# Optimization experiments

Measured on AMD Instinct MI355X. Metric: run time of the kernel, lower is better.

## Reference

```python
import jax, jax.numpy as jnp
import numpy as np

B_, L, DM = 2, 2048, 1024
DI, N, K, R = 2048, 16, 4, 64  # d_inner, d_state, d_conv, dt_rank


def setup_inputs() -> dict:
    key = jax.random.key(0)
    ks = jax.random.split(key, 8)
    return {
        "x": jax.random.normal(ks[0], (B_, L, DM), jnp.float32),
        "W_in": jax.random.normal(ks[1], (DM, 2 * DI), jnp.float32) * 0.02,
        "w_conv": jax.random.normal(ks[2], (DI, K), jnp.float32) * 0.1,
        "b_conv": jnp.zeros((DI,), jnp.float32),
        "W_x": jax.random.normal(ks[3], (DI, R + 2 * N), jnp.float32) * 0.02,
        "W_dt": jax.random.normal(ks[4], (R, DI), jnp.float32) * 0.02,
        "b_dt": jnp.full((DI,), -4.6, jnp.float32),  # softplus(b_dt) ~ 0.01 dt init
        "A_log": jnp.log(jnp.broadcast_to(jnp.arange(1, N + 1, dtype=jnp.float32), (DI, N))),
        "D": jnp.ones((DI,), jnp.float32),
        "W_out": jax.random.normal(ks[5], (DI, DM), jnp.float32) * 0.02,
        "gamma": jnp.ones((DM,), jnp.float32),
        "beta": jnp.zeros((DM,), jnp.float32),
    }


def reference(x, W_in, w_conv, b_conv, W_x, W_dt, b_dt, A_log, D, W_out, gamma, beta):
    Bb, Ll, Dm = x.shape
    Di, Kk = w_conv.shape
    Nn = A_log.shape[1]
    Rr = W_dt.shape[0]
    # in_proj -> (u, z)
    xz = x @ W_in  # [B,L,2*Di]
    u, z = jnp.split(xz, 2, axis=-1)
    # depthwise causal conv1d (kernel K, left pad K-1) + SiLU
    up = jnp.pad(u, ((0, 0), (Kk - 1, 0), (0, 0)))
    conv = b_conv + sum(up[:, k:k + Ll, :] * w_conv[:, k] for k in range(Kk))
    u = jax.nn.silu(conv)  # [B,L,Di]
    # x_proj -> dt, B, C
    dbc = u @ W_x
    dt, Bm, Cm = dbc[..., :Rr], dbc[..., Rr:Rr + Nn], dbc[..., Rr + Nn:]
    delta = jax.nn.softplus(dt @ W_dt + b_dt)  # [B,L,Di]
    A = -jnp.exp(A_log)  # [Di,N]

    def step(h, inputs):
        d_t, B_t, C_t, u_t = inputs  # [B,Di],[B,N],[B,N],[B,Di]
        dA = jnp.exp(d_t[..., None] * A)            # [B,Di,N]
        h = h * dA + (d_t * u_t)[..., None] * B_t[:, None, :]
        y = jnp.einsum('bdn,bn->bd', h, C_t)
        return h, y

    h0 = jnp.zeros((Bb, Di, Nn), x.dtype)
    _, ys = jax.lax.scan(step, h0, (delta.transpose(1, 0, 2), Bm.transpose(1, 0, 2),
                                    Cm.transpose(1, 0, 2), u.transpose(1, 0, 2)))
    y = ys.transpose(1, 0, 2)        # [B,L,Di]
    y = y + u * D                    # skip term
    y = y * jax.nn.silu(z)           # gate
    out = y @ W_out                  # [B,L,Dm]
    # LayerNorm
    mu = out.mean(-1, keepdims=True)
    var = ((out - mu) ** 2).mean(-1, keepdims=True)
    out = (out - mu) * jax.lax.rsqrt(var + 1e-5) * gamma + beta
    # dropout p=0 -> identity; residual
    return out + x
```

## Files before the change

kernel.cpp:

```cpp
#include <hip/hip_runtime.h>
#include <math.h>

#define L_SEQ 2048
#define DMOD  1024
#define DIN   2048
#define NBATCH 2
#define NTOK  (NBATCH * L_SEQ)
#define NST   16
#define RRANK 64
#define LOG2E 1.44269504088896f

#define GCHUNK 64
#define CLEN   (L_SEQ / GCHUNK)
#define SCHUNK 8
#define NSTAGE (CLEN / SCHUNK)

#define G4_KS   4
#define G4_KC   (2048 / G4_KS)
#define G2_KS   16
#define G2_KC   (2048 / G2_KS)

typedef __attribute__((ext_vector_type(8))) short  short8;
typedef __attribute__((ext_vector_type(4))) float  f32x4;

__device__ __forceinline__ ushort f2bf(float f) {
    unsigned u = __float_as_uint(f);
    u += 0x7fffu + ((u >> 16) & 1u);
    return (ushort)(u >> 16);
}
__device__ __forceinline__ float bf2f(ushort u) {
    return __uint_as_float(((unsigned)u) << 16);
}
__device__ __forceinline__ float fexp2(float x) {
    return __builtin_amdgcn_exp2f(x);
}

__device__ __forceinline__ void gload16(const ushort* g, ushort* l) {
    __builtin_amdgcn_global_load_lds(
        (const __attribute__((address_space(1))) unsigned int*)g,
        (__attribute__((address_space(3))) unsigned int*)l,
        16, 0, 0);
}

__device__ __forceinline__ void cast_body(
    const float* __restrict__ src, ushort* __restrict__ dst, int bid, int tid)
{
    int i = (bid * 256 + tid) * 8;
    float4 a = *(const float4*)(src + i);
    float4 b = *(const float4*)(src + i + 4);
    ushort4 o0 = make_ushort4(f2bf(a.x), f2bf(a.y), f2bf(a.z), f2bf(a.w));
    ushort4 o1 = make_ushort4(f2bf(b.x), f2bf(b.y), f2bf(b.z), f2bf(b.w));
    *(ushort4*)(dst + i)     = o0;
    *(ushort4*)(dst + i + 4) = o1;
}

__device__ __forceinline__ void tcast_body(
    const float* __restrict__ src, ushort* __restrict__ dst,
    int R, int C, int bx, int by, int tid)
{
    __shared__ float t[32][33];
    int tx = tid & 31;
    int ty = tid >> 5;
    int c0 = bx * 32;
    int r0 = by * 32;
    #pragma unroll
    for (int i = 0; i < 4; ++i)
        t[ty + i * 8][tx] = src[(size_t)(r0 + ty + i * 8) * C + c0 + tx];
    __syncthreads();
    #pragma unroll
    for (int i = 0; i < 4; ++i)
        dst[(size_t)(c0 + ty + i * 8) * R + r0 + tx] = f2bf(t[tx][ty + i * 8]);
}

__global__ __launch_bounds__(256) void prep_k(
    const float* __restrict__ x, const float* __restrict__ W_in,
    const float* __restrict__ W_dt, const float* __restrict__ W_x,
    const float* __restrict__ W_out,
    ushort* __restrict__ xb, ushort* __restrict__ Wib,
    ushort* __restrict__ Wdtb, ushort* __restrict__ Wxb,
    ushort* __restrict__ Wob)
{
    int bid = blockIdx.x, tid = threadIdx.x;
    if (bid < 2048) {
        cast_body(x, xb, bid, tid);
    } else if (bid < 6144) {
        int t = bid - 2048;
        tcast_body(W_in, Wib, 1024, 4096, t & 127, t >> 7, tid);
    } else if (bid < 6272) {
        int t = bid - 6144;
        tcast_body(W_dt, Wdtb, 64, 2048, t & 63, t >> 6, tid);
    } else if (bid < 6464) {
        int t = bid - 6272;
        tcast_body(W_x, Wxb, 2048, 96, t % 3, t / 3, tid);
    } else {
        int t = bid - 6464;
        tcast_body(W_out, Wob, 2048, 1024, t & 31, t >> 5, tid);
    }
}

__global__ __launch_bounds__(512, 2) void gemm8p(
    const ushort* __restrict__ A,
    const ushort* __restrict__ Bt,
    ushort* __restrict__ C,
    int K, int kslice, int ldc, size_t zstride)
{
    __shared__ ushort As[4][8192];
    __shared__ ushort Bs[4][8192];

    const int tid  = threadIdx.x;
    const int wave = tid >> 6;
    const int lane = tid & 63;
    const int wr   = wave >> 2;
    const int wc   = wave & 3;

    const int gx = gridDim.x;
    int flat = blockIdx.y * gx + blockIdx.x;
    const int cpx = (gx * gridDim.y) >> 3;
    flat = (flat & 7) * cpx + (flat >> 3);
    const int bx = flat % gx;
    const int by = flat / gx;
    const int m0 = by * 256;
    const int n0 = bx * 256;
    const int kbeg = blockIdx.z * kslice;
    const int NS   = kslice >> 5;

    const int rr  = tid >> 2;
    const int gsw = ((tid & 3) ^ ((rr >> 1) & 3)) * 8;
    const ushort* a0 = A  + (size_t)(m0 + rr)        * K + kbeg + gsw;
    const ushort* a1 = A  + (size_t)(m0 + 128 + rr)  * K + kbeg + gsw;
    const ushort* b0 = Bt + (size_t)(n0 + rr)        * K + kbeg + gsw;
    const ushort* b1 = Bt + (size_t)(n0 + 128 + rr)  * K + kbeg + gsw;
    ushort* asw = &As[0][0] + wave * 512;
    ushort* bsw = &Bs[0][0] + wave * 512;

    #define STAGE(s_) do { const int sl_ = (s_) & 3; const int ko_ = (s_) * 32; \
        gload16(a0 + ko_, asw + sl_ * 8192);                                     \
        gload16(a1 + ko_, asw + sl_ * 8192 + 4096);                              \
        gload16(b0 + ko_, bsw + sl_ * 8192);                                     \
        gload16(b1 + ko_, bsw + sl_ * 8192 + 4096); } while (0)

    const int lr  = lane & 15;
    const int swr = ((lane >> 4) ^ ((lr >> 1) & 3)) * 8;

    f32x4 acc[8][4];
    #pragma unroll
    for (int i = 0; i < 8; ++i)
        #pragma unroll
        for (int j = 0; j < 4; ++j)
            acc[i][j] = (f32x4){0.f, 0.f, 0.f, 0.f};

    STAGE(0); STAGE(1); STAGE(2);

    for (int s = 0; s < NS; ++s) {
        if (s + 2 < NS)
            asm volatile("s_waitcnt vmcnt(8) lgkmcnt(0)" ::: "memory");
        else if (s + 1 < NS)
            asm volatile("s_waitcnt vmcnt(4) lgkmcnt(0)" ::: "memory");
        else
            asm volatile("s_waitcnt vmcnt(0) lgkmcnt(0)" ::: "memory");
        asm volatile("s_barrier" ::: "memory");
        if (s + 3 < NS) STAGE(s + 3);

        const ushort* Ab = &As[s & 3][0];
        const ushort* Bb = &Bs[s & 3][0];
        short8 af[8], bfr[4];
        #pragma unroll
        for (int j = 0; j < 4; ++j)
            bfr[j] = *(const short8*)&Bb[(wc * 64 + j * 16 + lr) * 32 + swr];
        #pragma unroll
        for (int i = 0; i < 8; ++i)
            af[i] = *(const short8*)&Ab[(wr * 128 + i * 16 + lr) * 32 + swr];

        __builtin_amdgcn_s_setprio(1);
        #pragma unroll
        for (int i = 0; i < 8; ++i)
            #pragma unroll
            for (int j = 0; j < 4; ++j)
                acc[i][j] = __builtin_amdgcn_mfma_f32_16x16x32_bf16(
                    af[i], bfr[j], acc[i][j], 0, 0, 0);
        __builtin_amdgcn_s_setprio(0);
    }
    #undef STAGE

    ushort* Cp = C + (size_t)blockIdx.z * zstride;
    const int rb = m0 + wr * 128 + ((lane >> 4) << 2);
    const int cb = n0 + wc * 64 + lr;
    #pragma unroll
    for (int i = 0; i < 8; ++i)
        #pragma unroll
        for (int j = 0; j < 4; ++j)
            #pragma unroll
            for (int r = 0; r < 4; ++r)
                Cp[(size_t)(rb + i * 16 + r) * ldc + cb + j * 16] =
                    f2bf(acc[i][j][r]);
}

template<int EPI, int OBF>
__global__ __launch_bounds__(256) void gemm_mfma(
    const ushort* __restrict__ A,
    const ushort* __restrict__ Bt,
    void* __restrict__ Cv,
    int M, int N, int K, int ldc, const float* __restrict__ bias)
{
    __shared__ ushort As[128 * 32];
    __shared__ ushort Bs[128 * 32];

    const int tid  = threadIdx.x;
    const int wave = tid >> 6;
    const int lane = tid & 63;
    const int wm   = (wave & 1) * 64;
    const int wn   = (wave >> 1) * 64;
    const int m0   = blockIdx.y * 128;
    const int n0   = blockIdx.x * 128;

    const int srow = lane >> 2;
    const int sg   = (lane & 3) ^ ((srow >> 1) & 3);
    const ushort* gA0 = A  + (size_t)(m0 + wave * 32 + srow)      * K + sg * 8;
    const ushort* gA1 = A  + (size_t)(m0 + wave * 32 + 16 + srow) * K + sg * 8;
    const ushort* gB0 = Bt + (size_t)(n0 + wave * 32 + srow)      * K + sg * 8;
    const ushort* gB1 = Bt + (size_t)(n0 + wave * 32 + 16 + srow) * K + sg * 8;
    ushort* lA0 = As + (wave * 32)      * 32;
    ushort* lA1 = As + (wave * 32 + 16) * 32;
    ushort* lB0 = Bs + (wave * 32)      * 32;
    ushort* lB1 = Bs + (wave * 32 + 16) * 32;

    const int lrow = lane & 15;
    const int swr  = ((lane >> 4) ^ ((lrow >> 1) & 3)) * 8;

    f32x4 acc[4][4];
    #pragma unroll
    for (int i = 0; i < 4; ++i)
        #pragma unroll
        for (int j = 0; j < 4; ++j)
            acc[i][j] = (f32x4){0.f, 0.f, 0.f, 0.f};

    for (int k0 = 0; k0 < K; k0 += 32) {
        __syncthreads();
        gload16(gA0 + k0, lA0);
        gload16(gA1 + k0, lA1);
        gload16(gB0 + k0, lB0);
        gload16(gB1 + k0, lB1);
        __syncthreads();

        short8 af[4], bfr[4];
        #pragma unroll
        for (int i = 0; i < 4; ++i) {
            af[i]  = *(const short8*)&As[(wm + i * 16 + lrow) * 32 + swr];
            bfr[i] = *(const short8*)&Bs[(wn + i * 16 + lrow) * 32 + swr];
        }
        #pragma unroll
        for (int i = 0; i < 4; ++i)
            #pragma unroll
            for (int j = 0; j < 4; ++j)
                acc[i][j] = __builtin_amdgcn_mfma_f32_16x16x32_bf16(
                    af[i], bfr[j], acc[i][j], 0, 0, 0);
    }

    const int rb = m0 + wm + ((lane >> 4) << 2);
    const int cb = n0 + wn + lrow;
    #pragma unroll
    for (int i = 0; i < 4; ++i)
        #pragma unroll
        for (int j = 0; j < 4; ++j)
            #pragma unroll
            for (int r = 0; r < 4; ++r) {
                float v = acc[i][j][r];
                int col = cb + j * 16;
                if (EPI == 1) {
                    v += bias[col];
                    v = (v > 20.f) ? v : log1pf(__expf(v));
                }
                size_t off = (size_t)(rb + i * 16 + r) * ldc + col;
                if (OBF) ((ushort*)Cv)[off] = f2bf(v);
                else     ((float*)Cv)[off]  = v;
            }
}

__global__ __launch_bounds__(256) void gemm2_mfma(
    const ushort* __restrict__ A,
    const ushort* __restrict__ Bt,
    float* __restrict__ part)
{
    __shared__ ushort As[128 * 32];
    __shared__ ushort Bs[128 * 32];

    const int K = 2048;
    const int tid  = threadIdx.x;
    const int wave = tid >> 6;
    const int lane = tid & 63;
    const int wm   = (wave & 1) * 64;
    const int wn   = (wave >> 1) * 64;
    const int m0   = blockIdx.x * 128;
    const int ks   = blockIdx.z;

    const int srow = lane >> 2;
    const int sg   = (lane & 3) ^ ((srow >> 1) & 3);
    int rB0 = wave * 32 + srow;      if (rB0 > 95) rB0 = 95;
    int rB1 = wave * 32 + 16 + srow; if (rB1 > 95) rB1 = 95;
    const ushort* gA0 = A  + (size_t)(m0 + wave * 32 + srow)      * K + sg * 8;
    const ushort* gA1 = A  + (size_t)(m0 + wave * 32 + 16 + srow) * K + sg * 8;
    const ushort* gB0 = Bt + (size_t)rB0 * K + sg * 8;
    const ushort* gB1 = Bt + (size_t)rB1 * K + sg * 8;
    ushort* lA0 = As + (wave * 32)      * 32;
    ushort* lA1 = As + (wave * 32 + 16) * 32;
    ushort* lB0 = Bs + (wave * 32)      * 32;
    ushort* lB1 = Bs + (wave * 32 + 16) * 32;

    const int lrow = lane & 15;
    const int swr  = ((lane >> 4) ^ ((lrow >> 1) & 3)) * 8;

    f32x4 acc[4][4];
    #pragma unroll
    for (int i = 0; i < 4; ++i)
        #pragma unroll
        for (int j = 0; j < 4; ++j)
            acc[i][j] = (f32x4){0.f, 0.f, 0.f, 0.f};

    const int kbeg = ks * G2_KC, kend = kbeg + G2_KC;
    for (int k0 = kbeg; k0 < kend; k0 += 32) {
        __syncthreads();
        gload16(gA0 + k0, lA0);
        gload16(gA1 + k0, lA1);
        gload16(gB0 + k0, lB0);
        gload16(gB1 + k0, lB1);
        __syncthreads();

        short8 af[4], bfr[4];
        #pragma unroll
        for (int i = 0; i < 4; ++i) {
            af[i]  = *(const short8*)&As[(wm + i * 16 + lrow) * 32 + swr];
            bfr[i] = *(const short8*)&Bs[(wn + i * 16 + lrow) * 32 + swr];
        }
        #pragma unroll
        for (int i = 0; i < 4; ++i)
            #pragma unroll
            for (int j = 0; j < 4; ++j)
                acc[i][j] = __builtin_amdgcn_mfma_f32_16x16x32_bf16(
                    af[i], bfr[j], acc[i][j], 0, 0, 0);
    }

    float* po = part + (size_t)ks * NTOK * 96;
    const int rb = m0 + wm + ((lane >> 4) << 2);
    const int cb = wn + lrow;
    #pragma unroll
    for (int i = 0; i < 4; ++i)
        #pragma unroll
        for (int j = 0; j < 4; ++j) {
            int col = cb + j * 16;
            if (col < 96) {
                #pragma unroll
                for (int r = 0; r < 4; ++r)
                    po[(size_t)(rb + i * 16 + r) * 96 + col] = acc[i][j][r];
            }
        }
}

__global__ __launch_bounds__(256) void gemm2_reduce_dt(
    const float* __restrict__ part, float* __restrict__ dbc,
    ushort* __restrict__ dtb)
{
    int i = (blockIdx.x * 256 + threadIdx.x) * 4;
    float4 s = *(const float4*)(part + i);
    #pragma unroll
    for (int ks = 1; ks < G2_KS; ++ks) {
        float4 v = *(const float4*)(part + (size_t)ks * NTOK * 96 + i);
        s.x += v.x; s.y += v.y; s.z += v.z; s.w += v.w;
    }
    *(float4*)(dbc + i) = s;
    int col = i % 96;
    if (col < RRANK) {
        int row = i / 96;
        ushort* q = dtb + (size_t)row * RRANK + col;
        q[0] = f2bf(s.x); q[1] = f2bf(s.y); q[2] = f2bf(s.z); q[3] = f2bf(s.w);
    }
}

__global__ __launch_bounds__(256) void conv_silu_k(
    const ushort* __restrict__ xzb, const float* __restrict__ w_conv,
    const float* __restrict__ b_conv, ushort* __restrict__ ub)
{
    int idx   = blockIdx.x * 256 + threadIdx.x;
    int d     = idx & (DIN - 1);
    int token = idx >> 11;
    int t     = token & (L_SEQ - 1);

    float acc = b_conv[d];
    #pragma unroll
    for (int k = 0; k < 4; ++k) {
        int tt = t - 3 + k;
        if (tt >= 0)
            acc += bf2f(xzb[(size_t)(token - 3 + k) * 4096 + d]) * w_conv[d * 4 + k];
    }
    float s = acc / (1.f + expf(-acc));
    ub[(size_t)token * DIN + d] = f2bf(s);
}

__global__ __launch_bounds__(64) void scan_part1(
    const float* __restrict__ dlt,
    const ushort* __restrict__ ub,
    const float* __restrict__ dbc,
    const float* __restrict__ A_log,
    float* __restrict__ c_out,
    float* __restrict__ dsum_out)
{
    int chunk = blockIdx.x & 63;
    int dg    = (blockIdx.x >> 6) & 31;
    int b     = blockIdx.x >> 11;
    int tid   = threadIdx.x;
    int d     = dg * 64 + tid;

    __shared__ float sB[SCHUNK][16];

    float Al[NST];
    const float4* pA = (const float4*)(A_log + (size_t)d * NST);
    #pragma unroll
    for (int q = 0; q < 4; ++q) {
        float4 a = pA[q];
        Al[q*4+0] = -__expf(a.x) * LOG2E;
        Al[q*4+1] = -__expf(a.y) * LOG2E;
        Al[q*4+2] = -__expf(a.z) * LOG2E;
        Al[q*4+3] = -__expf(a.w) * LOG2E;
    }

    float h[NST];
    #pragma unroll
    for (int n = 0; n < NST; ++n) h[n] = 0.f;
    float dsum = 0.f;

    const size_t tokbase = (size_t)b * L_SEQ + (size_t)chunk * CLEN;
    const float*  pD = dlt + tokbase * 2048 + d;
    const ushort* pU = ub  + tokbase * 2048 + d;
    const float*  pB = dbc + tokbase * 96 + RRANK;

    float rd[2][SCHUNK], ru[2][SCHUNK], rb[2][2];

    #pragma unroll
    for (int i = 0; i < SCHUNK; ++i) {
        rd[0][i] = pD[(size_t)i * 2048];
        ru[0][i] = bf2f(pU[(size_t)i * 2048]);
    }
    #pragma unroll
    for (int i = 0; i < 2; ++i) {
        int e = i * 64 + tid;
        rb[0][i] = pB[(size_t)(e >> 4) * 96 + (e & 15)];
    }

    #pragma unroll
    for (int st = 0; st < NSTAGE; ++st) {
        const int cur = st & 1, nxt = cur ^ 1;
        #pragma unroll
        for (int i = 0; i < 2; ++i) {
            int e = i * 64 + tid;
            sB[e >> 4][e & 15] = rb[cur][i];
        }
        if (st + 1 < NSTAGE) {
            const size_t to = (size_t)(st + 1) * SCHUNK;
            #pragma unroll
            for (int i = 0; i < SCHUNK; ++i) {
                rd[nxt][i] = pD[(to + i) * 2048];
                ru[nxt][i] = bf2f(pU[(to + i) * 2048]);
            }
            #pragma unroll
            for (int i = 0; i < 2; ++i) {
                int e = i * 64 + tid;
                rb[nxt][i] = pB[(to + (e >> 4)) * 96 + (e & 15)];
            }
        }
        #pragma unroll
        for (int s = 0; s < SCHUNK; ++s) {
            float delta = rd[cur][s];
            float du    = delta * ru[cur][s];
            dsum += delta;
            #pragma unroll
            for (int q = 0; q < 4; ++q) {
                float4 bq = *(const float4*)&sB[s][q * 4];
                h[q*4+0] = h[q*4+0] * fexp2(delta * Al[q*4+0]) + du * bq.x;
                h[q*4+1] = h[q*4+1] * fexp2(delta * Al[q*4+1]) + du * bq.y;
                h[q*4+2] = h[q*4+2] * fexp2(delta * Al[q*4+2]) + du * bq.z;
                h[q*4+3] = h[q*4+3] * fexp2(delta * Al[q*4+3]) + du * bq.w;
            }
        }
    }

    size_t base = (((size_t)b * DIN + d) * GCHUNK + chunk) * NST;
    #pragma unroll
    for (int q = 0; q < 4; ++q)
        *(float4*)&c_out[base + q * 4] = make_float4(h[q*4], h[q*4+1], h[q*4+2], h[q*4+3]);
    dsum_out[((size_t)b * DIN + d) * GCHUNK + chunk] = dsum;
}

__global__ __launch_bounds__(256) void scan_part2(
    float* __restrict__ cbuf,
    const float* __restrict__ dsum_in,
    const float* __restrict__ A_log)
{
    int idx = blockIdx.x * 256 + threadIdx.x;
    int n   = idx & 15;
    int d   = (idx >> 4) & (DIN - 1);
    int b   = idx >> 15;

    float Al = -__expf(A_log[(size_t)d * NST + n]) * LOG2E;
    size_t cb = ((size_t)b * DIN + d) * GCHUNK;

    float h = 0.f;
    for (int ch = 0; ch < GCHUNK; ++ch) {
        size_t o = (cb + ch) * NST + n;
        float c  = cbuf[o];
        float dA = fexp2(Al * dsum_in[cb + ch]);
        cbuf[o]  = h;
        h = h * dA + c;
    }
}

__global__ __launch_bounds__(64) void scan_part3(
    const float* __restrict__ dlt,
    const ushort* __restrict__ xzb,
    ushort* __restrict__ ub,
    const float* __restrict__ dbc,
    const float* __restrict__ A_log,
    const float* __restrict__ Dp,
    const float* __restrict__ h_start)
{
    int chunk = blockIdx.x & 63;
    int dg    = (blockIdx.x >> 6) & 31;
    int b     = blockIdx.x >> 11;
    int tid   = threadIdx.x;
    int d     = dg * 64 + tid;

    __shared__ float sBC[SCHUNK][32];

    float Al[NST];
    const float4* pA = (const float4*)(A_log + (size_t)d * NST);
    #pragma unroll
    for (int q = 0; q < 4; ++q) {
        float4 a = pA[q];
        Al[q*4+0] = -__expf(a.x) * LOG2E;
        Al[q*4+1] = -__expf(a.y) * LOG2E;
        Al[q*4+2] = -__expf(a.z) * LOG2E;
        Al[q*4+3] = -__expf(a.w) * LOG2E;
    }
    float Dd = Dp[d];

    float h[NST];
    size_t hb = (((size_t)b * DIN + d) * GCHUNK + chunk) * NST;
    #pragma unroll
    for (int q = 0; q < 4; ++q) {
        float4 v = *(const float4*)&h_start[hb + q * 4];
        h[q*4] = v.x; h[q*4+1] = v.y; h[q*4+2] = v.z; h[q*4+3] = v.w;
    }

    const size_t tokbase = (size_t)b * L_SEQ + (size_t)chunk * CLEN;
    const float*  pD = dlt + tokbase * 2048 + d;
    const ushort* pZ = xzb + tokbase * 4096 + 2048 + d;
    ushort*       pU = ub  + tokbase * 2048 + d;
    const float*  pB = dbc + tokbase * 96 + RRANK;

    float rd[2][SCHUNK], ru[2][SCHUNK], rz[2][SCHUNK], rb[2][4];

    #pragma unroll
    for (int i = 0; i < SCHUNK; ++i) {
        rd[0][i] = pD[(size_t)i * 2048];
        ru[0][i] = bf2f(pU[(size_t)i * 2048]);
        rz[0][i] = bf2f(pZ[(size_t)i * 4096]);
    }
    #pragma unroll
    for (int i = 0; i < 4; ++i) {
        int e = i * 64 + tid;
        rb[0][i] = pB[(size_t)(e >> 5) * 96 + (e & 31)];
    }

    #pragma unroll
    for (int st = 0; st < NSTAGE; ++st) {
        const int cur = st & 1, nxt = cur ^ 1;
        #pragma unroll
        for (int i = 0; i < 4; ++i) {
            int e = i * 64 + tid;
            sBC[e >> 5][e & 31] = rb[cur][i];
        }
        if (st + 1 < NSTAGE) {
            const size_t to = (size_t)(st + 1) * SCHUNK;
            #pragma unroll
            for (int i = 0; i < SCHUNK; ++i) {
                rd[nxt][i] = pD[(to + i) * 2048];
                ru[nxt][i] = bf2f(pU[(to + i) * 2048]);
                rz[nxt][i] = bf2f(pZ[(to + i) * 4096]);
            }
            #pragma unroll
            for (int i = 0; i < 4; ++i) {
                int e = i * 64 + tid;
                rb[nxt][i] = pB[(to + (e >> 5)) * 96 + (e & 31)];
            }
        }
        #pragma unroll
        for (int s = 0; s < SCHUNK; ++s) {
            float delta = rd[cur][s];
            float u     = ru[cur][s];
            float du    = delta * u;
            float y = 0.f;
            #pragma unroll
            for (int q = 0; q < 4; ++q) {
                float4 bq = *(const float4*)&sBC[s][q * 4];
                float4 cq = *(const float4*)&sBC[s][16 + q * 4];
                h[q*4+0] = h[q*4+0] * fexp2(delta * Al[q*4+0]) + du * bq.x; y += h[q*4+0] * cq.x;
                h[q*4+1] = h[q*4+1] * fexp2(delta * Al[q*4+1]) + du * bq.y; y += h[q*4+1] * cq.y;
                h[q*4+2] = h[q*4+2] * fexp2(delta * Al[q*4+2]) + du * bq.z; y += h[q*4+2] * cq.z;
                h[q*4+3] = h[q*4+3] * fexp2(delta * Al[q*4+3]) + du * bq.w; y += h[q*4+3] * cq.w;
            }
            float z  = rz[cur][s];
            float sz = z / (1.f + __expf(-z));
            pU[((size_t)st * SCHUNK + s) * 2048] = f2bf((y + u * Dd) * sz);
        }
    }
}

__global__ __launch_bounds__(256) void ln4_k(
    const ushort* __restrict__ part,
    const float* __restrict__ x,
    const float* __restrict__ gamma, const float* __restrict__ beta,
    float* __restrict__ out)
{
    int row = blockIdx.x;
    int tid = threadIdx.x;
    const size_t off = (size_t)row * DMOD + tid * 4;

    float4 v = {0.f, 0.f, 0.f, 0.f};
    #pragma unroll
    for (int ks = 0; ks < G4_KS; ++ks) {
        ushort4 p = *(const ushort4*)(part + (size_t)ks * NTOK * DMOD + off);
        v.x += bf2f(p.x); v.y += bf2f(p.y); v.z += bf2f(p.z); v.w += bf2f(p.w);
    }

    float s  = v.x + v.y + v.z + v.w;
    float s2 = v.x * v.x + v.y * v.y + v.z * v.z + v.w * v.w;
    #pragma unroll
    for (int off2 = 32; off2 > 0; off2 >>= 1) {
        s  += __shfl_down(s, off2);
        s2 += __shfl_down(s2, off2);
    }
    __shared__ float ws[4], ws2[4];
    int wave = tid >> 6, lane = tid & 63;
    if (lane == 0) { ws[wave] = s; ws2[wave] = s2; }
    __syncthreads();
    if (tid == 0) {
        float ts = 0.f, ts2 = 0.f;
        #pragma unroll
        for (int w = 0; w < 4; ++w) { ts += ws[w]; ts2 += ws2[w]; }
        ws[0] = ts; ws2[0] = ts2;
    }
    __syncthreads();
    float mu  = ws[0] * (1.f / DMOD);
    float var = ws2[0] * (1.f / DMOD) - mu * mu;
    float rs  = rsqrtf(var + 1e-5f);

    float4 g  = ((const float4*)gamma)[tid];
    float4 be = ((const float4*)beta)[tid];
    float4 xr = *(const float4*)(x + off);
    float4 o;
    o.x = (v.x - mu) * rs * g.x + be.x + xr.x;
    o.y = (v.y - mu) * rs * g.y + be.y + xr.y;
    o.z = (v.z - mu) * rs * g.z + be.z + xr.z;
    o.w = (v.w - mu) * rs * g.w + be.w + xr.w;
    *(float4*)(out + off) = o;
}

extern "C" void kernel_launch(void* const* d_in, const int* in_sizes, int n_in,
                              void* d_out, int out_size, void* d_ws, size_t ws_size,
                              hipStream_t stream)
{
    const float* x      = (const float*)d_in[0];
    const float* W_in   = (const float*)d_in[1];
    const float* w_conv = (const float*)d_in[2];
    const float* b_conv = (const float*)d_in[3];
    const float* W_x    = (const float*)d_in[4];
    const float* W_dt   = (const float*)d_in[5];
    const float* b_dt   = (const float*)d_in[6];
    const float* A_log  = (const float*)d_in[7];
    const float* Dp     = (const float*)d_in[8];
    const float* W_out  = (const float*)d_in[9];
    const float* gamma  = (const float*)d_in[10];
    const float* beta   = (const float*)d_in[11];
    float* out = (float*)d_out;

    char* ws = (char*)d_ws;
    const size_t MB = 1024 * 1024;
    ushort* xzb   = (ushort*)(ws);
    ushort* ub    = (ushort*)(ws + 32 * MB);
    float*  dlt   = (float*)(ws + 48 * MB);
    float*  dbc   = (float*)(ws + 80 * MB);
    ushort* Wdtb  = (ushort*)(ws + 81 * MB + 512 * 1024);
    ushort* Wxb   = (ushort*)(ws + 81 * MB + 768 * 1024);
    float*  dsum  = (float*)(ws + 82 * MB + 256 * 1024);
    float*  c_buf = (float*)(ws + 84 * MB);
    ushort* xb    = (ushort*)(ws + 84 * MB);
    ushort* Wib   = (ushort*)(ws + 92 * MB);
    float*  g2part = (float*)(ws + 84 * MB);
    ushort* dtb   = (ushort*)(ws + 108 * MB);
    ushort* Wob   = (ushort*)(ws + 109 * MB);
    ushort* g4part = (ushort*)(ws + 48 * MB);

    dim3 blk(256);

    prep_k<<<dim3(8512), blk, 0, stream>>>(x, W_in, W_dt, W_x, W_out,
                                           xb, Wib, Wdtb, Wxb, Wob);
    gemm8p<<<dim3(16, 16, 1), dim3(512), 0, stream>>>(
        xb, Wib, xzb, 1024, 1024, 4096, 0);
    conv_silu_k<<<dim3(NTOK * DIN / 256), blk, 0, stream>>>(xzb, w_conv, b_conv, ub);
    gemm2_mfma<<<dim3(32, 1, G2_KS), blk, 0, stream>>>(ub, Wxb, g2part);
    gemm2_reduce_dt<<<dim3(NTOK * 96 / 4 / 256), blk, 0, stream>>>(g2part, dbc, dtb);
    gemm_mfma<1, 0><<<dim3(16, 32), blk, 0, stream>>>(
        dtb, Wdtb, dlt, 4096, 2048, 64, 2048, b_dt);
    scan_part1<<<dim3(NBATCH * 32 * GCHUNK), dim3(64), 0, stream>>>(
        dlt, ub, dbc, A_log, c_buf, dsum);
    scan_part2<<<dim3(NBATCH * DIN * NST / 256), blk, 0, stream>>>(
        c_buf, dsum, A_log);
    scan_part3<<<dim3(NBATCH * 32 * GCHUNK), dim3(64), 0, stream>>>(
        dlt, xzb, ub, dbc, A_log, Dp, c_buf);
    gemm8p<<<dim3(4, 16, G4_KS), dim3(512), 0, stream>>>(
        ub, Wob, g4part, 2048, G4_KC, DMOD, (size_t)NTOK * DMOD);
    ln4_k<<<dim3(NTOK), blk, 0, stream>>>(g4part, x, gamma, beta, out);
}
```

Before: 352.4 us.

## Restructure 256x256 bf16 GEMM mainloop into double-buffered 64-K tiles with interleaved loads

Replaces the 4-slot, 32-wide K pipeline in gemm8p with a two-buffer scheme over 64-wide K tiles. Each tile is split into four phases that interleave LDS fragment reads, global-to-LDS staging of the next tile, and half-tile MFMA blocks, separated by explicit barriers and sched_barriers. Holding only half the A fragments at a time lowers register pressure. The aim is to overlap memory traffic with MFMA issue in a ping-pong style, at the cost of many more barriers per tile. The global load swizzle also changes, and it must still match the LDS read swizzle.

```diff
diff --git a/kernel.cpp b/kernel.cpp
--- a/kernel.cpp
+++ b/kernel.cpp
@@ -104,8 +104,7 @@
     ushort* __restrict__ C,
     int K, int kslice, int ldc, size_t zstride)
 {
-    __shared__ ushort As[4][8192];
-    __shared__ ushort Bs[4][8192];
+    __shared__ ushort lds[65536];
 
     const int tid  = threadIdx.x;
     const int wave = tid >> 6;
@@ -122,26 +121,31 @@
     const int m0 = by * 256;
     const int n0 = bx * 256;
     const int kbeg = blockIdx.z * kslice;
-    const int NS   = kslice >> 5;
+    const int NT   = kslice >> 6;
 
     const int rr  = tid >> 2;
-    const int gsw = ((tid & 3) ^ ((rr >> 1) & 3)) * 8;
+    const int gsw = ((tid & 3) ^ ((tid >> 3) & 3)) * 8;
     const ushort* a0 = A  + (size_t)(m0 + rr)        * K + kbeg + gsw;
     const ushort* a1 = A  + (size_t)(m0 + 128 + rr)  * K + kbeg + gsw;
     const ushort* b0 = Bt + (size_t)(n0 + rr)        * K + kbeg + gsw;
     const ushort* b1 = Bt + (size_t)(n0 + 128 + rr)  * K + kbeg + gsw;
-    ushort* asw = &As[0][0] + wave * 512;
-    ushort* bsw = &Bs[0][0] + wave * 512;
-
-    #define STAGE(s_) do { const int sl_ = (s_) & 3; const int ko_ = (s_) * 32; \
-        gload16(a0 + ko_, asw + sl_ * 8192);                                     \
-        gload16(a1 + ko_, asw + sl_ * 8192 + 4096);                              \
-        gload16(b0 + ko_, bsw + sl_ * 8192);                                     \
-        gload16(b1 + ko_, bsw + sl_ * 8192 + 4096); } while (0)
+
+    #define STAGE_U(op_, ks_, kt_, bf_) do {                                   \
+        const int ko_ = (kt_) * 64 + (ks_) * 32;                               \
+        ushort* l_ = lds + (bf_) * 32768 + (op_) * 16384 + (ks_) * 8192        \
+                         + wave * 512;                                         \
+        if ((op_) == 0) { gload16(a0 + ko_, l_); gload16(a1 + ko_, l_ + 4096); }\
+        else            { gload16(b0 + ko_, l_); gload16(b1 + ko_, l_ + 4096); }\
+    } while (0)
 
     const int lr  = lane & 15;
     const int swr = ((lane >> 4) ^ ((lr >> 1) & 3)) * 8;
 
+    #define LDA(i_, ks_) (*(const short8*)&lds[buf * 32768 + (ks_) * 8192      \
+        + (wr * 128 + (i_) * 16 + lr) * 32 + swr])
+    #define LDB(j_, ks_) (*(const short8*)&lds[buf * 32768 + 16384             \
+        + (ks_) * 8192 + (wc * 64 + (j_) * 16 + lr) * 32 + swr])
+
     f32x4 acc[8][4];
     #pragma unroll
     for (int i = 0; i < 8; ++i)
@@ -149,38 +153,96 @@
         for (int j = 0; j < 4; ++j)
             acc[i][j] = (f32x4){0.f, 0.f, 0.f, 0.f};
 
-    STAGE(0); STAGE(1); STAGE(2);
-
-    for (int s = 0; s < NS; ++s) {
-        if (s + 2 < NS)
-            asm volatile("s_waitcnt vmcnt(8) lgkmcnt(0)" ::: "memory");
-        else if (s + 1 < NS)
-            asm volatile("s_waitcnt vmcnt(4) lgkmcnt(0)" ::: "memory");
-        else
-            asm volatile("s_waitcnt vmcnt(0) lgkmcnt(0)" ::: "memory");
-        asm volatile("s_barrier" ::: "memory");
-        if (s + 3 < NS) STAGE(s + 3);
-
-        const ushort* Ab = &As[s & 3][0];
-        const ushort* Bb = &Bs[s & 3][0];
-        short8 af[8], bfr[4];
-        #pragma unroll
-        for (int j = 0; j < 4; ++j)
-            bfr[j] = *(const short8*)&Bb[(wc * 64 + j * 16 + lr) * 32 + swr];
-        #pragma unroll
-        for (int i = 0; i < 8; ++i)
-            af[i] = *(const short8*)&Ab[(wr * 128 + i * 16 + lr) * 32 + swr];
-
+    STAGE_U(0, 0, 0, 0); STAGE_U(1, 0, 0, 0);
+    STAGE_U(0, 1, 0, 0); STAGE_U(1, 1, 0, 0);
+    asm volatile("s_waitcnt vmcnt(4)" ::: "memory");
+    __builtin_amdgcn_s_barrier();
+
+    short8 a_[4], b_[4];
+
+    for (int t = 0; t < NT; ++t) {
+        const int buf = t & 1, nb = buf ^ 1;
+        const bool st = (t + 1 < NT);
+
+        #pragma unroll
+        for (int i = 0; i < 4; ++i) a_[i] = LDA(i, 0);
+        #pragma unroll
+        for (int j = 0; j < 4; ++j) b_[j] = LDB(j, 0);
+        if (st) STAGE_U(0, 0, t + 1, nb);
+        __builtin_amdgcn_s_barrier();
+        asm volatile("s_waitcnt lgkmcnt(0)" ::: "memory");
+        __builtin_amdgcn_sched_barrier(0);
         __builtin_amdgcn_s_setprio(1);
         #pragma unroll
-        for (int i = 0; i < 8; ++i)
+        for (int i = 0; i < 4; ++i)
             #pragma unroll
             for (int j = 0; j < 4; ++j)
                 acc[i][j] = __builtin_amdgcn_mfma_f32_16x16x32_bf16(
-                    af[i], bfr[j], acc[i][j], 0, 0, 0);
+                    a_[i], b_[j], acc[i][j], 0, 0, 0);
         __builtin_amdgcn_s_setprio(0);
-    }
-    #undef STAGE
+        __builtin_amdgcn_s_barrier();
+
+        #pragma unroll
+        for (int i = 0; i < 4; ++i) a_[i] = LDA(4 + i, 0);
+        if (st) {
+            STAGE_U(1, 0, t + 1, nb);
+            asm volatile("s_waitcnt vmcnt(4)" ::: "memory");
+        } else {
+            asm volatile("s_waitcnt vmcnt(0)" ::: "memory");
+        }
+        __builtin_amdgcn_s_barrier();
+        asm volatile("s_waitcnt lgkmcnt(0)" ::: "memory");
+        __builtin_amdgcn_sched_barrier(0);
+        __builtin_amdgcn_s_setprio(1);
+        #pragma unroll
+        for (int i = 0; i < 4; ++i)
+            #pragma unroll
+            for (int j = 0; j < 4; ++j)
+                acc[4 + i][j] = __builtin_amdgcn_mfma_f32_16x16x32_bf16(
+                    a_[i], b_[j], acc[4 + i][j], 0, 0, 0);
+        __builtin_amdgcn_s_setprio(0);
+        __builtin_amdgcn_s_barrier();
+
+        #pragma unroll
+        for (int i = 0; i < 4; ++i) a_[i] = LDA(i, 1);
+        #pragma unroll
+        for (int j = 0; j < 4; ++j) b_[j] = LDB(j, 1);
+        if (st) STAGE_U(0, 1, t + 1, nb);
+        __builtin_amdgcn_s_barrier();
+        asm volatile("s_waitcnt lgkmcnt(0)" ::: "memory");
+        __builtin_amdgcn_sched_barrier(0);
+        __builtin_amdgcn_s_setprio(1);
+        #pragma unroll
+        for (int i = 0; i < 4; ++i)
+            #pragma unroll
+            for (int j = 0; j < 4; ++j)
+                acc[i][j] = __builtin_amdgcn_mfma_f32_16x16x32_bf16(
+                    a_[i], b_[j], acc[i][j], 0, 0, 0);
+        __builtin_amdgcn_s_setprio(0);
+        __builtin_amdgcn_s_barrier();
+
+        #pragma unroll
+        for (int i = 0; i < 4; ++i) a_[i] = LDA(4 + i, 1);
+        if (st) {
+            STAGE_U(1, 1, t + 1, nb);
+            asm volatile("s_waitcnt vmcnt(4)" ::: "memory");
+        }
+        __builtin_amdgcn_s_barrier();
+        asm volatile("s_waitcnt lgkmcnt(0)" ::: "memory");
+        __builtin_amdgcn_sched_barrier(0);
+        __builtin_amdgcn_s_setprio(1);
+        #pragma unroll
+        for (int i = 0; i < 4; ++i)
+            #pragma unroll
+            for (int j = 0; j < 4; ++j)
+                acc[4 + i][j] = __builtin_amdgcn_mfma_f32_16x16x32_bf16(
+                    a_[i], b_[j], acc[4 + i][j], 0, 0, 0);
+        __builtin_amdgcn_s_setprio(0);
+        __builtin_amdgcn_s_barrier();
+    }
+    #undef STAGE_U
+    #undef LDA
+    #undef LDB
 
     ushort* Cp = C + (size_t)blockIdx.z * zstride;
     const int rb = m0 + wr * 128 + ((lane >> 4) << 2);
```

Measured after the change: 336.1 us. 1.05x faster.
